# Kernel optimization log

Measured on AMD Instinct MI355X. Metric: run time of the kernel, lower is better.

Reference implementation:

```python
import jax, jax.numpy as jnp
import numpy as np

LAYERS = 5      # lstm_layers
H = 1           # lstm_hidden_size
IN = 21         # 9 (rot) + 6 (v) + 6 (u)
NEG = 0.1       # LeakyReLU negative slope
EPS = 1e-5      # BatchNorm1d eps


def _lstm_cell(x, h, c, w_ih, w_hh):
    # torch gate order: i, f, g, o ; no biases (lstm_bias=False)
    gates = x @ w_ih.T + h @ w_hh.T              # [k, 4H]
    i, f, g, o = jnp.split(gates, 4, axis=-1)
    i = jax.nn.sigmoid(i)
    f = jax.nn.sigmoid(f)
    g = jnp.tanh(g)
    o = jax.nn.sigmoid(o)
    c_new = f * c + i * g
    h_new = o * jnp.tanh(c_new)
    return h_new, c_new


def _bn_train(z, gamma, beta):
    # BatchNorm1d in training mode: batch stats, biased variance
    m = z.mean(axis=0)
    var = z.var(axis=0)
    return gamma * (z - m) / jnp.sqrt(var + EPS) + beta


def setup_inputs() -> dict:
    key = jax.random.key(0)
    ks = jax.random.split(key, 14)
    k, T = 65536, 32
    s = 0.2  # init scale, roughly torch uniform(-1/sqrt(H)) magnitude
    inp = {
        "r": jax.random.normal(ks[0], (k, T, 9), jnp.float32),
        "v": jax.random.normal(ks[1], (k, T, 6), jnp.float32),
        "u": jax.random.normal(ks[2], (k, T, 6), jnp.float32),
        # LSTM weights: layer 0 sees IN features, layers 1..4 see H
        "w_ih0": jax.random.normal(ks[3], (4 * H, IN), jnp.float32) * s,
        "w_ih_rest": jax.random.normal(ks[4], (LAYERS - 1, 4 * H, H), jnp.float32) * s,
        "w_hh": jax.random.normal(ks[5], (LAYERS, 4 * H, H), jnp.float32) * s,
        # FC head: Linear(H,32,no bias) -> BN -> LReLU -> Linear(32,32) -> BN -> LReLU -> Linear(32,6)
        "W1": jax.random.normal(ks[6], (32, H), jnp.float32) * s,
        "g1": jnp.ones((32,), jnp.float32),
        "b1": jnp.zeros((32,), jnp.float32),
        "W2": jax.random.normal(ks[7], (32, 32), jnp.float32) * s,
        "g2": jnp.ones((32,), jnp.float32),
        "b2": jnp.zeros((32,), jnp.float32),
        "W3": jax.random.normal(ks[8], (6, 32), jnp.float32) * s,
    }
    return inp


def reference(r, v, u, w_ih0, w_ih_rest, w_hh, W1, g1, b1, W2, g2, b2, W3):
    x = jnp.concatenate([r, v, u], axis=-1)          # [k, T, 21]
    k = x.shape[0]
    h0 = jnp.zeros((LAYERS, k, H), x.dtype)
    c0 = jnp.zeros((LAYERS, k, H), x.dtype)
    xs = jnp.swapaxes(x, 0, 1)                       # [T, k, 21]

    def step(carry, xt):
        h, c = carry
        hs, cs = [], []
        layer_in = xt
        for l in range(LAYERS):
            w_ih = w_ih0 if l == 0 else w_ih_rest[l - 1]
            hl, cl = _lstm_cell(layer_in, h[l], c[l], w_ih, w_hh[l])
            hs.append(hl)
            cs.append(cl)
            layer_in = hl
        return (jnp.stack(hs), jnp.stack(cs)), layer_in  # top-layer output

    (hT, cT), outs = jax.lax.scan(step, (h0, c0), xs)    # outs: [T, k, H]

    # fc applied to out[:, 0] -> first timestep of top layer
    y = outs[0]                                          # [k, H]
    y = jax.nn.leaky_relu(_bn_train(y @ W1.T, g1, b1), NEG)
    y = jax.nn.leaky_relu(_bn_train(y @ W2.T, g2, b2), NEG)
    dv = y @ W3.T                                        # [k, 6]
    return dv[:, None], hT, cT
```

## Files before the change

### kernel.cpp

```cpp
#include <hip/hip_runtime.h>
#include <math.h>

#define T 32
#define NEGS 0.1f
#define EPS 1e-5f
#define NREG 33
#define NH (3 * NREG)


__device__ __forceinline__ float rcp_fast(float x) { return __builtin_amdgcn_rcpf(x); }
__device__ __forceinline__ float sigm(float x) { return rcp_fast(1.0f + __expf(-x)); }
__device__ __forceinline__ float tanh_fast(float x) {
    float t = __expf(2.0f * fabsf(x));
    float r = 1.0f - 2.0f * rcp_fast(t + 1.0f);
    return copysignf(r, x);
}
__device__ __forceinline__ float lrelu(float x) { return x > 0.0f ? x : NEGS * x; }

__device__ __forceinline__ void bn1_ab(const float* __restrict__ W1,
                                       const float* __restrict__ g1,
                                       const float* __restrict__ b1,
                                       float my, float vy, int j,
                                       float& a, float& b, float& tau, int& flip)
{
    float wj = W1[j];
    a = g1[j] * wj * rsqrtf(fmaf(wj * wj, vy, EPS));
    b = b1[j];
    if (a > 0.0f)      { tau = my - b / a; flip = 0; }
    else if (a < 0.0f) { tau = my - b / a; flip = 1; }
    else               { tau = (b > 0.0f ? -__builtin_inff() : __builtin_inff()); flip = 0; }
}

__device__ __forceinline__ void reduce_stats(const double* __restrict__ bSums, int nb, int k,
                                             float* outMy, float* outVy)
{
    const int tid = threadIdx.x;
    double sy = 0.0, sq = 0.0;
    for (int i = tid; i < nb; i += 256) { sy += bSums[2 * i]; sq += bSums[2 * i + 1]; }
#pragma unroll
    for (int off = 32; off; off >>= 1) {
        sy += __shfl_down(sy, off);
        sq += __shfl_down(sq, off);
    }
    __shared__ double dS[4], dQ[4];
    const int wid = tid >> 6, lane = tid & 63;
    if (lane == 0) { dS[wid] = sy; dQ[wid] = sq; }
    __syncthreads();
    if (tid == 0) {
        double tS = dS[0] + dS[1] + dS[2] + dS[3];
        double tQ = dQ[0] + dQ[1] + dQ[2] + dQ[3];
        float my = (float)(tS / k);
        *outMy = my;
        *outVy = (float)(tQ / k) - my * my;
    }
    __syncthreads();
}

__global__ __launch_bounds__(256)
void gates_kernel(const float* __restrict__ r, const float* __restrict__ v,
                  const float* __restrict__ u, const float* __restrict__ wih0,
                  float4* __restrict__ xg, int k)
{
    __shared__ float rS[2304], vS[1536], uS[1536];
    __shared__ float gT[32 * 36];
    const int tid = threadIdx.x;
    const int s0 = blockIdx.x * 8;
    const int sl = tid >> 5, t = tid & 31;

    const float4* rG = (const float4*)(r + (size_t)s0 * 288);
    const float4* vG = (const float4*)(v + (size_t)s0 * 192);
    const float4* uG = (const float4*)(u + (size_t)s0 * 192);
    for (int i = tid; i < 576; i += 256) ((float4*)rS)[i] = rG[i];
    for (int i = tid; i < 384; i += 256) ((float4*)vS)[i] = vG[i];
    for (int i = tid; i < 384; i += 256) ((float4*)uS)[i] = uG[i];

    float wi0[4][21];
#pragma unroll
    for (int g = 0; g < 4; ++g)
#pragma unroll
        for (int j = 0; j < 21; ++j) wi0[g][j] = wih0[g * 21 + j];

    __syncthreads();

    float x[21];
#pragma unroll
    for (int j = 0; j < 9; ++j) x[j] = rS[sl * 288 + t * 9 + j];
#pragma unroll
    for (int j = 0; j < 6; ++j) x[9 + j] = vS[sl * 192 + t * 6 + j];
#pragma unroll
    for (int j = 0; j < 6; ++j) x[15 + j] = uS[sl * 192 + t * 6 + j];

    float4 g4;
    float* gp = (float*)&g4;
#pragma unroll
    for (int g = 0; g < 4; ++g) {
        float acc = 0.f;
#pragma unroll
        for (int j = 0; j < 21; ++j) acc = fmaf(wi0[g][j], x[j], acc);
        gp[g] = acc;
    }
    *(float4*)&gT[t * 36 + sl * 4] = g4;
    __syncthreads();

    const int tG = tid >> 3, j = tid & 7;
    float4 val = *(const float4*)&gT[tG * 36 + j * 4];
    xg[(size_t)tG * k + s0 + j] = val;
}

__global__ __launch_bounds__(256, 1)
void recur_kernel(const float4* __restrict__ xg, const float* __restrict__ wihr,
                  const float* __restrict__ whhp, float* __restrict__ out,
                  double* __restrict__ bSums, float* __restrict__ wsy, int k)
{
    const int s = blockIdx.x * 256 + threadIdx.x;

    float wir[4][4];
#pragma unroll
    for (int l = 0; l < 4; ++l)
#pragma unroll
        for (int g = 0; g < 4; ++g) wir[l][g] = wihr[l * 4 + g];
    float whh[5][4];
#pragma unroll
    for (int l = 0; l < 5; ++l)
#pragma unroll
        for (int g = 0; g < 4; ++g) whh[l][g] = whhp[l * 4 + g];

    float4 gbuf[T];
#pragma unroll
    for (int t = 0; t < T; ++t) gbuf[t] = xg[(size_t)t * k + s];

    float h[5] = {0.f, 0.f, 0.f, 0.f, 0.f};
    float c[5] = {0.f, 0.f, 0.f, 0.f, 0.f};
    float y0 = 0.f;

#pragma unroll
    for (int t = 0; t < T; ++t) {
        const float4 G = gbuf[t];
        float a0 = fmaf(whh[0][0], h[0], G.x);
        float a1 = fmaf(whh[0][1], h[0], G.y);
        float a2 = fmaf(whh[0][2], h[0], G.z);
        float a3 = fmaf(whh[0][3], h[0], G.w);
        {
            float ii = sigm(a0), ff = sigm(a1);
            float gg = tanh_fast(a2), oo = sigm(a3);
            c[0] = ff * c[0] + ii * gg;
            h[0] = oo * tanh_fast(c[0]);
        }
        float xin = h[0];
#pragma unroll
        for (int l = 1; l < 5; ++l) {
            float b0 = fmaf(wir[l - 1][0], xin, whh[l][0] * h[l]);
            float b1 = fmaf(wir[l - 1][1], xin, whh[l][1] * h[l]);
            float b2 = fmaf(wir[l - 1][2], xin, whh[l][2] * h[l]);
            float b3 = fmaf(wir[l - 1][3], xin, whh[l][3] * h[l]);
            float ii = sigm(b0), ff = sigm(b1);
            float gg = tanh_fast(b2), oo = sigm(b3);
            c[l] = ff * c[l] + ii * gg;
            h[l] = oo * tanh_fast(c[l]);
            xin = h[l];
        }
        if (t == 0) y0 = h[4];
    }

#pragma unroll
    for (int l = 0; l < 5; ++l) {
        out[(size_t)6 * k + (size_t)l * k + s] = h[l];
        out[(size_t)11 * k + (size_t)l * k + s] = c[l];
    }
    wsy[s] = y0;

    float ys = y0, yq = y0 * y0;
#pragma unroll
    for (int off = 32; off; off >>= 1) {
        ys += __shfl_down(ys, off);
        yq += __shfl_down(yq, off);
    }
    __shared__ float pS[4], pQ[4];
    const int wid = threadIdx.x >> 6, lane = threadIdx.x & 63;
    if (lane == 0) { pS[wid] = ys; pQ[wid] = yq; }
    __syncthreads();
    if (threadIdx.x == 0) {
        bSums[2 * blockIdx.x] = (double)(pS[0] + pS[1] + pS[2] + pS[3]);
        bSums[2 * blockIdx.x + 1] = (double)(pQ[0] + pQ[1] + pQ[2] + pQ[3]);
    }
}

__global__ __launch_bounds__(256, 1)
void lstm_fused(const float* __restrict__ r, const float* __restrict__ v,
                const float* __restrict__ u,
                const float* __restrict__ wih0, const float* __restrict__ wihr,
                const float* __restrict__ whhp,
                float* __restrict__ out, double* __restrict__ bSums,
                float* __restrict__ wsy, int k)
{
    const int s = blockIdx.x * 256 + threadIdx.x;
    float wi0[4][21];
#pragma unroll
    for (int g = 0; g < 4; ++g)
#pragma unroll
        for (int j = 0; j < 21; ++j) wi0[g][j] = wih0[g * 21 + j];
    float wir[4][4];
#pragma unroll
    for (int l = 0; l < 4; ++l)
#pragma unroll
        for (int g = 0; g < 4; ++g) wir[l][g] = wihr[l * 4 + g];
    float whh[5][4];
#pragma unroll
    for (int l = 0; l < 5; ++l)
#pragma unroll
        for (int g = 0; g < 4; ++g) whh[l][g] = whhp[l * 4 + g];

    const float4* r4 = reinterpret_cast<const float4*>(r + (size_t)s * (T * 9));
    const float4* v4 = reinterpret_cast<const float4*>(v + (size_t)s * (T * 6));
    const float4* u4 = reinterpret_cast<const float4*>(u + (size_t)s * (T * 6));

    float h[5] = {0.f, 0.f, 0.f, 0.f, 0.f};
    float c[5] = {0.f, 0.f, 0.f, 0.f, 0.f};
    float y0 = 0.f;

    for (int t0 = 0; t0 < T; t0 += 4) {
        const int cb = t0 >> 2;
        float4 rb[9], vb[6], ub[6];
#pragma unroll
        for (int q = 0; q < 9; ++q) rb[q] = r4[cb * 9 + q];
#pragma unroll
        for (int q = 0; q < 6; ++q) vb[q] = v4[cb * 6 + q];
#pragma unroll
        for (int q = 0; q < 6; ++q) ub[q] = u4[cb * 6 + q];
        float rf[36], vf[24], uf[24];
#pragma unroll
        for (int q = 0; q < 9; ++q) {
            rf[4 * q] = rb[q].x; rf[4 * q + 1] = rb[q].y;
            rf[4 * q + 2] = rb[q].z; rf[4 * q + 3] = rb[q].w;
        }
#pragma unroll
        for (int q = 0; q < 6; ++q) {
            vf[4 * q] = vb[q].x; vf[4 * q + 1] = vb[q].y;
            vf[4 * q + 2] = vb[q].z; vf[4 * q + 3] = vb[q].w;
            uf[4 * q] = ub[q].x; uf[4 * q + 1] = ub[q].y;
            uf[4 * q + 2] = ub[q].z; uf[4 * q + 3] = ub[q].w;
        }
#pragma unroll
        for (int dt = 0; dt < 4; ++dt) {
            float x[21];
#pragma unroll
            for (int j = 0; j < 9; ++j) x[j] = rf[dt * 9 + j];
#pragma unroll
            for (int j = 0; j < 6; ++j) x[9 + j] = vf[dt * 6 + j];
#pragma unroll
            for (int j = 0; j < 6; ++j) x[15 + j] = uf[dt * 6 + j];
            float gt[4];
#pragma unroll
            for (int g = 0; g < 4; ++g) {
                float a = whh[0][g] * h[0];
#pragma unroll
                for (int j = 0; j < 21; ++j) a = fmaf(wi0[g][j], x[j], a);
                gt[g] = a;
            }
            {
                float ii = sigm(gt[0]), ff = sigm(gt[1]);
                float gg = tanh_fast(gt[2]), oo = sigm(gt[3]);
                c[0] = ff * c[0] + ii * gg;
                h[0] = oo * tanh_fast(c[0]);
            }
            float xin = h[0];
#pragma unroll
            for (int l = 1; l < 5; ++l) {
                float b0 = fmaf(wir[l - 1][0], xin, whh[l][0] * h[l]);
                float b1 = fmaf(wir[l - 1][1], xin, whh[l][1] * h[l]);
                float b2 = fmaf(wir[l - 1][2], xin, whh[l][2] * h[l]);
                float b3 = fmaf(wir[l - 1][3], xin, whh[l][3] * h[l]);
                float ii = sigm(b0), ff = sigm(b1);
                float gg = tanh_fast(b2), oo = sigm(b3);
                c[l] = ff * c[l] + ii * gg;
                h[l] = oo * tanh_fast(c[l]);
                xin = h[l];
            }
            if (t0 + dt == 0) y0 = h[4];
        }
    }
#pragma unroll
    for (int l = 0; l < 5; ++l) {
        out[(size_t)6 * k + (size_t)l * k + s] = h[l];
        out[(size_t)11 * k + (size_t)l * k + s] = c[l];
    }
    wsy[s] = y0;
    float ys = y0, yq = y0 * y0;
#pragma unroll
    for (int off = 32; off; off >>= 1) {
        ys += __shfl_down(ys, off);
        yq += __shfl_down(yq, off);
    }
    __shared__ float pS[4], pQ[4];
    const int wid = threadIdx.x >> 6, lane = threadIdx.x & 63;
    if (lane == 0) { pS[wid] = ys; pQ[wid] = yq; }
    __syncthreads();
    if (threadIdx.x == 0) {
        bSums[2 * blockIdx.x] = (double)(pS[0] + pS[1] + pS[2] + pS[3]);
        bSums[2 * blockIdx.x + 1] = (double)(pQ[0] + pQ[1] + pQ[2] + pQ[3]);
    }
}

__global__ __launch_bounds__(256)
void hist_kernel(const float* __restrict__ W1, const float* __restrict__ g1,
                 const float* __restrict__ b1, const double* __restrict__ bSums, int nb,
                 float* __restrict__ bHist, const float* __restrict__ wsy, int k)
{
    __shared__ float sMy, sVy;
    __shared__ float sTau[32];
    __shared__ float sH[NH];
    const int tid = threadIdx.x;
    reduce_stats(bSums, nb, k, &sMy, &sVy);
    if (tid < NH) sH[tid] = 0.f;
    if (tid < 32) {
        float a, b, tau; int flip;
        bn1_ab(W1, g1, b1, sMy, sVy, tid, a, b, tau, flip);
        sTau[tid] = tau;
    }
    __syncthreads();
    const float my = sMy;
    const int stride = gridDim.x * 256;
    for (int s = blockIdx.x * 256 + tid; s < k; s += stride) {
        const float y = wsy[s];
        const float yc = y - my;
        int rgn = 0;
#pragma unroll
        for (int j = 0; j < 32; ++j) rgn += (y > sTau[j]) ? 1 : 0;
        atomicAdd(&sH[rgn], 1.0f);
        atomicAdd(&sH[NREG + rgn], yc);
        atomicAdd(&sH[2 * NREG + rgn], yc * yc);
    }
    __syncthreads();
    if (tid < NH) bHist[blockIdx.x * NH + tid] = sH[tid];
}

__global__ __launch_bounds__(256)
void tables_kernel(const float* __restrict__ W1, const float* __restrict__ g1,
                   const float* __restrict__ b1, const float* __restrict__ W2,
                   const float* __restrict__ g2, const float* __restrict__ b2,
                   const double* __restrict__ bSums, int nb,
                   const float* __restrict__ bHist, int nhb,
                   float* __restrict__ gPQ, int k)
{
    __shared__ float sMy, sVy;
    __shared__ float sA[32], sB[32], sTau[32];
    __shared__ int sRank[32], sFlip[32];
    __shared__ float sS0[NREG], sS1[NREG], sS2[NREG];
    __shared__ float sW2[1024];
    __shared__ float sSumY1[32];
    __shared__ float sM[1024];
    __shared__ float sI2[32], sM2v[32], sB2[32];
    const int tid = threadIdx.x;

    reduce_stats(bSums, nb, k, &sMy, &sVy);
    for (int i = tid; i < 1024; i += 256) sW2[i] = W2[i];
    if (tid < NH) {
        float acc = 0.f;
        for (int bk = 0; bk < nhb; ++bk) acc += bHist[bk * NH + tid];
        if (tid < NREG)           sS0[tid] = acc;
        else if (tid < 2 * NREG)  sS1[tid - NREG] = acc;
        else                      sS2[tid - 2 * NREG] = acc;
    }
    if (tid < 32) {
        float a, b, tau; int flip;
        bn1_ab(W1, g1, b1, sMy, sVy, tid, a, b, tau, flip);
        sA[tid] = a; sB[tid] = b; sTau[tid] = tau; sFlip[tid] = flip;
        sB2[tid] = b2[tid];
    }
    __syncthreads();
    if (tid < 32) {
        int rk = 0;
        float tj = sTau[tid];
#pragma unroll
        for (int l = 0; l < 32; ++l)
            rk += (sTau[l] < tj || (sTau[l] == tj && l < tid)) ? 1 : 0;
        sRank[tid] = rk;
    }
    __syncthreads();
    if (tid < 32) {
        const int rk = sRank[tid], fl = sFlip[tid];
        const float a = sA[tid], b = sB[tid];
        float acc = 0.f;
        for (int rg = 0; rg < NREG; ++rg) {
            float m = (((rk < rg) ? 1 : 0) != fl) ? 1.0f : NEGS;
            acc += m * (a * sS1[rg] + b * sS0[rg]);
        }
        sSumY1[tid] = acc;
    }
    for (int p = tid; p < 1024; p += 256) {
        const int j = p >> 5, l = p & 31;
        const int rj = sRank[j], fj = sFlip[j];
        const int rl = sRank[l], flp = sFlip[l];
        const float aj = sA[j], bj = sB[j], al = sA[l], bl = sB[l];
        const float caa = aj * al, cab = aj * bl + al * bj, cbb = bj * bl;
        float acc = 0.f;
        for (int rg = 0; rg < NREG; ++rg) {
            float mj = (((rj < rg) ? 1 : 0) != fj) ? 1.0f : NEGS;
            float ml = (((rl < rg) ? 1 : 0) != flp) ? 1.0f : NEGS;
            acc += mj * ml * (caa * sS2[rg] + cab * sS1[rg] + cbb * sS0[rg]);
        }
        sM[p] = acc;
    }
    __syncthreads();
    if (tid < 32) {
        const int i = tid;
        float s2 = 0.f, ss2 = 0.f;
#pragma unroll
        for (int j = 0; j < 32; ++j) {
            float wij = sW2[i * 32 + j];
            s2 = fmaf(wij, sSumY1[j], s2);
            float tj = 0.f;
#pragma unroll
            for (int l = 0; l < 32; ++l) tj = fmaf(sW2[i * 32 + l], sM[j * 32 + l], tj);
            ss2 = fmaf(wij, tj, ss2);
        }
        float m2 = s2 / k;
        float v2 = ss2 / k - m2 * m2;
        sM2v[i] = m2;
        sI2[i] = g2[i] * rsqrtf(v2 + EPS);
    }
    __syncthreads();
    for (int idx = tid; idx < NREG * 32; idx += 256) {
        const int rg = idx >> 5, i = idx & 31;
        float Ai = 0.f, Bi = 0.f;
#pragma unroll
        for (int j = 0; j < 32; ++j) {
            float m = (((sRank[j] < rg) ? 1 : 0) != sFlip[j]) ? 1.0f : NEGS;
            float w = sW2[i * 32 + j] * m;
            Ai = fmaf(w, sA[j], Ai);
            Bi = fmaf(w, sB[j], Bi);
        }
        gPQ[idx] = sI2[i] * Ai;
        gPQ[NREG * 32 + idx] = sI2[i] * (Bi - sM2v[i]) + sB2[i];
    }
    if (tid < 32) gPQ[2 * NREG * 32 + tid] = sTau[tid];
    if (tid == 0) gPQ[2 * NREG * 32 + 32] = sMy;
}

__global__ __launch_bounds__(256)
void final_kernel(const float* __restrict__ W3, const float* __restrict__ wsy,
                  const float* __restrict__ gPQ, float* __restrict__ out, int k)
{
    __shared__ float sTau[32], sW3[192], sMy;
    __shared__ float sP[NREG][33], sQ[NREG][33];
    const int tid = threadIdx.x;
    for (int idx = tid; idx < NREG * 32; idx += 256) {
        const int rg = idx >> 5, i = idx & 31;
        sP[rg][i] = gPQ[idx];
        sQ[rg][i] = gPQ[NREG * 32 + idx];
    }
    if (tid < 192) sW3[tid] = W3[tid];
    if (tid < 32) sTau[tid] = gPQ[2 * NREG * 32 + tid];
    if (tid == 0) sMy = gPQ[2 * NREG * 32 + 32];
    __syncthreads();
    const int s = blockIdx.x * 256 + tid;
    const float y = wsy[s];
    const float yc = y - sMy;
    int rgn = 0;
#pragma unroll
    for (int j = 0; j < 32; ++j) rgn += (y > sTau[j]) ? 1 : 0;
    float dv[6] = {0.f, 0.f, 0.f, 0.f, 0.f, 0.f};
#pragma unroll
    for (int i = 0; i < 32; ++i) {
        float y2 = lrelu(fmaf(sP[rgn][i], yc, sQ[rgn][i]));
#pragma unroll
        for (int m = 0; m < 6; ++m) dv[m] = fmaf(sW3[m * 32 + i], y2, dv[m]);
    }
#pragma unroll
    for (int m = 0; m < 6; ++m) out[(size_t)s * 6 + m] = dv[m];
}

extern "C" void kernel_launch(void* const* d_in, const int* in_sizes, int n_in,
                              void* d_out, int out_size, void* d_ws, size_t ws_size,
                              hipStream_t stream)
{
    const float* r    = (const float*)d_in[0];
    const float* v    = (const float*)d_in[1];
    const float* u    = (const float*)d_in[2];
    const float* wih0 = (const float*)d_in[3];
    const float* wihr = (const float*)d_in[4];
    const float* whhp = (const float*)d_in[5];
    const float* W1   = (const float*)d_in[6];
    const float* g1v  = (const float*)d_in[7];
    const float* b1v  = (const float*)d_in[8];
    const float* W2   = (const float*)d_in[9];
    const float* g2v  = (const float*)d_in[10];
    const float* b2v  = (const float*)d_in[11];
    const float* W3   = (const float*)d_in[12];

    const int k = in_sizes[0] / (T * 9);
    const int blocks = k / 256;
    const int HB = 64;
    float* out = (float*)d_out;

    double* bSums = (double*)d_ws;
    float* bHist  = (float*)((char*)d_ws + 4096);
    float* wsy    = (float*)((char*)d_ws + 32768);
    const size_t xg_off = 32768 + (size_t)k * 4;
    const size_t need = xg_off + (size_t)k * T * 16 + 2176 * 4;

    float* gPQ;
    if (ws_size >= need) {
        float4* xg = (float4*)((char*)d_ws + xg_off);
        gPQ = (float*)((char*)d_ws + xg_off + (size_t)k * T * 16);
        gates_kernel<<<k / 8, 256, 0, stream>>>(r, v, u, wih0, xg, k);
        recur_kernel<<<blocks, 256, 0, stream>>>(xg, wihr, whhp, out, bSums, wsy, k);
    } else {
        gPQ = (float*)((char*)d_ws + xg_off);
        lstm_fused<<<blocks, 256, 0, stream>>>(r, v, u, wih0, wihr, whhp, out, bSums, wsy, k);
    }
    hist_kernel<<<HB, 256, 0, stream>>>(W1, g1v, b1v, bSums, blocks, bHist, wsy, k);
    tables_kernel<<<1, 256, 0, stream>>>(W1, g1v, b1v, W2, g2v, b2v, bSums, blocks,
                                         bHist, HB, gPQ, k);
    final_kernel<<<blocks, 256, 0, stream>>>(W3, wsy, gPQ, out, k);
}
```

Measured before the change: 270.7 us.

## Make gates kernel persistent over 8 sample groups with register-prefetched double buffering

The gates kernel now handles 64 samples per block in 8 iterations instead of 8 samples per block. The next group's r/v/u data is prefetched into registers while the current group is computed, with double-buffered LDS. The goal is to hide global load latency and amortize the per-block load of the 84 weights. Barriers use a custom waitcnt-based LDS barrier. The trade-off is 8x fewer blocks and higher register pressure, which may reduce parallelism for latency hiding.

```diff
diff --git a/kernel.cpp b/kernel.cpp
--- a/kernel.cpp
+++ b/kernel.cpp
@@ -17,6 +17,13 @@
 }
 __device__ __forceinline__ float lrelu(float x) { return x > 0.0f ? x : NEGS * x; }
 
+__device__ __forceinline__ void lds_barrier() {
+    __asm__ volatile("" ::: "memory");
+    __builtin_amdgcn_s_waitcnt(0xC07F);
+    __builtin_amdgcn_s_barrier();
+    __asm__ volatile("" ::: "memory");
+}
+
 __device__ __forceinline__ void bn1_ab(const float* __restrict__ W1,
                                        const float* __restrict__ g1,
                                        const float* __restrict__ b1,
@@ -56,23 +63,15 @@
     __syncthreads();
 }
 
-__global__ __launch_bounds__(256)
+__global__ __launch_bounds__(256, 3)
 void gates_kernel(const float* __restrict__ r, const float* __restrict__ v,
                   const float* __restrict__ u, const float* __restrict__ wih0,
                   float4* __restrict__ xg, int k)
 {
-    __shared__ float rS[2304], vS[1536], uS[1536];
-    __shared__ float gT[32 * 36];
+    __shared__ float4 inS[2][1344];
+    __shared__ float4 gT[2][288];
     const int tid = threadIdx.x;
-    const int s0 = blockIdx.x * 8;
-    const int sl = tid >> 5, t = tid & 31;
-
-    const float4* rG = (const float4*)(r + (size_t)s0 * 288);
-    const float4* vG = (const float4*)(v + (size_t)s0 * 192);
-    const float4* uG = (const float4*)(u + (size_t)s0 * 192);
-    for (int i = tid; i < 576; i += 256) ((float4*)rS)[i] = rG[i];
-    for (int i = tid; i < 384; i += 256) ((float4*)vS)[i] = vG[i];
-    for (int i = tid; i < 384; i += 256) ((float4*)uS)[i] = uG[i];
+    const int s00 = blockIdx.x * 64;
 
     float wi0[4][21];
 #pragma unroll
@@ -80,31 +79,66 @@
 #pragma unroll
         for (int j = 0; j < 21; ++j) wi0[g][j] = wih0[g * 21 + j];
 
-    __syncthreads();
-
-    float x[21];
-#pragma unroll
-    for (int j = 0; j < 9; ++j) x[j] = rS[sl * 288 + t * 9 + j];
-#pragma unroll
-    for (int j = 0; j < 6; ++j) x[9 + j] = vS[sl * 192 + t * 6 + j];
-#pragma unroll
-    for (int j = 0; j < 6; ++j) x[15 + j] = uS[sl * 192 + t * 6 + j];
-
-    float4 g4;
-    float* gp = (float*)&g4;
-#pragma unroll
-    for (int g = 0; g < 4; ++g) {
-        float acc = 0.f;
-#pragma unroll
-        for (int j = 0; j < 21; ++j) acc = fmaf(wi0[g][j], x[j], acc);
-        gp[g] = acc;
-    }
-    *(float4*)&gT[t * 36 + sl * 4] = g4;
-    __syncthreads();
-
-    const int tG = tid >> 3, j = tid & 7;
-    float4 val = *(const float4*)&gT[tG * 36 + j * 4];
-    xg[(size_t)tG * k + s0 + j] = val;
+    float4 pre[6];
+    {
+        const int s0 = s00;
+        const float4* rG = (const float4*)(r + (size_t)s0 * 288);
+        const float4* vG = (const float4*)(v + (size_t)s0 * 192);
+        const float4* uG = (const float4*)(u + (size_t)s0 * 192);
+#pragma unroll
+        for (int j = 0; j < 6; ++j) {
+            int i = tid + j * 256;
+            if (i < 1344) pre[j] = (i < 576) ? rG[i] : (i < 960 ? vG[i - 576] : uG[i - 960]);
+        }
+    }
+
+    for (int g = 0; g < 8; ++g) {
+        const int buf = g & 1;
+        lds_barrier();
+#pragma unroll
+        for (int j = 0; j < 6; ++j) {
+            int i = tid + j * 256;
+            if (i < 1344) inS[buf][i] = pre[j];
+        }
+        if (g < 7) {
+            const int s0 = s00 + (g + 1) * 8;
+            const float4* rG = (const float4*)(r + (size_t)s0 * 288);
+            const float4* vG = (const float4*)(v + (size_t)s0 * 192);
+            const float4* uG = (const float4*)(u + (size_t)s0 * 192);
+#pragma unroll
+            for (int j = 0; j < 6; ++j) {
+                int i = tid + j * 256;
+                if (i < 1344) pre[j] = (i < 576) ? rG[i] : (i < 960 ? vG[i - 576] : uG[i - 960]);
+            }
+        }
+        lds_barrier();
+
+        const int sl = tid >> 5, t = tid & 31;
+        const float* bi = (const float*)&inS[buf][0];
+        float x[21];
+#pragma unroll
+        for (int j = 0; j < 9; ++j) x[j] = bi[sl * 288 + t * 9 + j];
+#pragma unroll
+        for (int j = 0; j < 6; ++j) x[9 + j] = bi[2304 + sl * 192 + t * 6 + j];
+#pragma unroll
+        for (int j = 0; j < 6; ++j) x[15 + j] = bi[3840 + sl * 192 + t * 6 + j];
+
+        float4 g4;
+        float* gp = (float*)&g4;
+#pragma unroll
+        for (int q = 0; q < 4; ++q) {
+            float acc = 0.f;
+#pragma unroll
+            for (int j = 0; j < 21; ++j) acc = fmaf(wi0[q][j], x[j], acc);
+            gp[q] = acc;
+        }
+        gT[buf][t * 9 + sl] = g4;
+        lds_barrier();
+
+        const int tG = tid >> 3, jj = tid & 7;
+        float4 val = gT[buf][tG * 9 + jj];
+        xg[(size_t)tG * k + s00 + g * 8 + jj] = val;
+    }
 }
 
 __global__ __launch_bounds__(256, 1)
@@ -503,7 +537,7 @@
     if (ws_size >= need) {
         float4* xg = (float4*)((char*)d_ws + xg_off);
         gPQ = (float*)((char*)d_ws + xg_off + (size_t)k * T * 16);
-        gates_kernel<<<k / 8, 256, 0, stream>>>(r, v, u, wih0, xg, k);
+        gates_kernel<<<k / 64, 256, 0, stream>>>(r, v, u, wih0, xg, k);
         recur_kernel<<<blocks, 256, 0, stream>>>(xg, wihr, whhp, out, bSums, wsy, k);
     } else {
         gPQ = (float*)((char*)d_ws + xg_off);
```

New measurement: 359.6 us. +32.8%, slower.

## Store precomputed input gates as fp16 in sequence-major layout

Applied to the files above, without the earlier changes.

The layer-0 input-gate projections are now stored as packed half-precision ushort4 instead of float4, halving the intermediate buffer traffic between the gates and recurrence kernels. The layout changes from time-major to sequence-major, so each recurrence thread reads its 32 timesteps contiguously. The gates kernel drops its shared-memory staging and transpose, and reads inputs directly with strided per-thread loads. The cost is fp16 rounding of gate pre-activations, which can slightly change results, plus uncoalesced direct global reads of inputs and per-thread strided reads in the recurrence.

```diff
diff --git a/kernel.cpp b/kernel.cpp
--- a/kernel.cpp
+++ b/kernel.cpp
@@ -1,4 +1,5 @@
 #include <hip/hip_runtime.h>
+#include <hip/hip_fp16.h>
 #include <math.h>
 
 #define T 32
@@ -59,20 +60,10 @@
 __global__ __launch_bounds__(256)
 void gates_kernel(const float* __restrict__ r, const float* __restrict__ v,
                   const float* __restrict__ u, const float* __restrict__ wih0,
-                  float4* __restrict__ xg, int k)
-{
-    __shared__ float rS[2304], vS[1536], uS[1536];
-    __shared__ float gT[32 * 36];
-    const int tid = threadIdx.x;
-    const int s0 = blockIdx.x * 8;
-    const int sl = tid >> 5, t = tid & 31;
-
-    const float4* rG = (const float4*)(r + (size_t)s0 * 288);
-    const float4* vG = (const float4*)(v + (size_t)s0 * 192);
-    const float4* uG = (const float4*)(u + (size_t)s0 * 192);
-    for (int i = tid; i < 576; i += 256) ((float4*)rS)[i] = rG[i];
-    for (int i = tid; i < 384; i += 256) ((float4*)vS)[i] = vG[i];
-    for (int i = tid; i < 384; i += 256) ((float4*)uS)[i] = uG[i];
+                  ushort4* __restrict__ xg, int k)
+{
+    const int idx = blockIdx.x * 256 + threadIdx.x;
+    const int s = idx >> 5, t = idx & 31;
 
     float wi0[4][21];
 #pragma unroll
@@ -80,35 +71,35 @@
 #pragma unroll
         for (int j = 0; j < 21; ++j) wi0[g][j] = wih0[g * 21 + j];
 
-    __syncthreads();
-
+    const float* rp = r + (size_t)s * 288 + t * 9;
+    const float* vp = v + (size_t)s * 192 + t * 6;
+    const float* up = u + (size_t)s * 192 + t * 6;
     float x[21];
 #pragma unroll
-    for (int j = 0; j < 9; ++j) x[j] = rS[sl * 288 + t * 9 + j];
-#pragma unroll
-    for (int j = 0; j < 6; ++j) x[9 + j] = vS[sl * 192 + t * 6 + j];
-#pragma unroll
-    for (int j = 0; j < 6; ++j) x[15 + j] = uS[sl * 192 + t * 6 + j];
-
-    float4 g4;
-    float* gp = (float*)&g4;
+    for (int j = 0; j < 9; ++j) x[j] = rp[j];
+#pragma unroll
+    for (int j = 0; j < 6; ++j) x[9 + j] = vp[j];
+#pragma unroll
+    for (int j = 0; j < 6; ++j) x[15 + j] = up[j];
+
+    float acc[4];
 #pragma unroll
     for (int g = 0; g < 4; ++g) {
-        float acc = 0.f;
-#pragma unroll
-        for (int j = 0; j < 21; ++j) acc = fmaf(wi0[g][j], x[j], acc);
-        gp[g] = acc;
-    }
-    *(float4*)&gT[t * 36 + sl * 4] = g4;
-    __syncthreads();
-
-    const int tG = tid >> 3, j = tid & 7;
-    float4 val = *(const float4*)&gT[tG * 36 + j * 4];
-    xg[(size_t)tG * k + s0 + j] = val;
+        float a = 0.f;
+#pragma unroll
+        for (int j = 0; j < 21; ++j) a = fmaf(wi0[g][j], x[j], a);
+        acc[g] = a;
+    }
+    ushort4 pk;
+    pk.x = __half_as_ushort(__float2half(acc[0]));
+    pk.y = __half_as_ushort(__float2half(acc[1]));
+    pk.z = __half_as_ushort(__float2half(acc[2]));
+    pk.w = __half_as_ushort(__float2half(acc[3]));
+    xg[idx] = pk;
 }
 
 __global__ __launch_bounds__(256, 1)
-void recur_kernel(const float4* __restrict__ xg, const float* __restrict__ wihr,
+void recur_kernel(const ushort4* __restrict__ xg, const float* __restrict__ wihr,
                   const float* __restrict__ whhp, float* __restrict__ out,
                   double* __restrict__ bSums, float* __restrict__ wsy, int k)
 {
@@ -125,9 +116,10 @@
 #pragma unroll
         for (int g = 0; g < 4; ++g) whh[l][g] = whhp[l * 4 + g];
 
-    float4 gbuf[T];
-#pragma unroll
-    for (int t = 0; t < T; ++t) gbuf[t] = xg[(size_t)t * k + s];
+    ushort4 gbuf[T];
+    const ushort4* gp = xg + (size_t)s * T;
+#pragma unroll
+    for (int t = 0; t < T; ++t) gbuf[t] = gp[t];
 
     float h[5] = {0.f, 0.f, 0.f, 0.f, 0.f};
     float c[5] = {0.f, 0.f, 0.f, 0.f, 0.f};
@@ -135,11 +127,11 @@
 
 #pragma unroll
     for (int t = 0; t < T; ++t) {
-        const float4 G = gbuf[t];
-        float a0 = fmaf(whh[0][0], h[0], G.x);
-        float a1 = fmaf(whh[0][1], h[0], G.y);
-        float a2 = fmaf(whh[0][2], h[0], G.z);
-        float a3 = fmaf(whh[0][3], h[0], G.w);
+        const ushort4 G = gbuf[t];
+        float a0 = fmaf(whh[0][0], h[0], __half2float(__ushort_as_half(G.x)));
+        float a1 = fmaf(whh[0][1], h[0], __half2float(__ushort_as_half(G.y)));
+        float a2 = fmaf(whh[0][2], h[0], __half2float(__ushort_as_half(G.z)));
+        float a3 = fmaf(whh[0][3], h[0], __half2float(__ushort_as_half(G.w)));
         {
             float ii = sigm(a0), ff = sigm(a1);
             float gg = tanh_fast(a2), oo = sigm(a3);
@@ -497,13 +489,13 @@
     float* bHist  = (float*)((char*)d_ws + 4096);
     float* wsy    = (float*)((char*)d_ws + 32768);
     const size_t xg_off = 32768 + (size_t)k * 4;
-    const size_t need = xg_off + (size_t)k * T * 16 + 2176 * 4;
+    const size_t need = xg_off + (size_t)k * T * 8 + 2176 * 4;
 
     float* gPQ;
     if (ws_size >= need) {
-        float4* xg = (float4*)((char*)d_ws + xg_off);
-        gPQ = (float*)((char*)d_ws + xg_off + (size_t)k * T * 16);
-        gates_kernel<<<k / 8, 256, 0, stream>>>(r, v, u, wih0, xg, k);
+        ushort4* xg = (ushort4*)((char*)d_ws + xg_off);
+        gPQ = (float*)((char*)d_ws + xg_off + (size_t)k * T * 8);
+        gates_kernel<<<(k * T) / 256, 256, 0, stream>>>(r, v, u, wih0, xg, k);
         recur_kernel<<<blocks, 256, 0, stream>>>(xg, wihr, whhp, out, bSums, wsy, k);
     } else {
         gPQ = (float*)((char*)d_ws + xg_off);
```

After: 266.4 us. No clear change (-1.6%).
